# Kernel optimization log

Hardware: AMD Instinct MI355X
Metric: run time of the kernel (lower is better)

Reference implementation:

```python
import jax, jax.numpy as jnp
import numpy as np

N, D, V = 4096, 1024, 50257


def setup_inputs() -> dict:
    key = jax.random.key(0)
    kx, kw, kt = jax.random.split(key, 3)
    x = jax.random.normal(kx, (N, D), dtype=jnp.float32)
    weight = jax.random.normal(kw, (V, D), dtype=jnp.float32) * 0.02
    target = jax.random.randint(kt, (N,), 0, V, dtype=jnp.int64)
    return {"x": x, "weight": weight, "target": target}


def reference(x, weight, target):
    # fused fc -> log_softmax -> nll_loss (mean reduction)
    logits = jnp.einsum("nd,vd->nv", x, weight)          # [N, V]
    logp = jax.nn.log_softmax(logits, axis=-1)            # stable log-softmax
    nll = -jnp.take_along_axis(logp, target[:, None].astype(jnp.int32), axis=-1)[:, 0]
    return jnp.mean(nll)
```

## Files before the change

kernel.cpp:

```cpp
#include <hip/hip_runtime.h>
#include <hip/hip_bf16.h>
#include <stdint.h>

#define NROWS 4096
#define DDIM  1024
#define VDIM  50257
#define VPAD  50304
#define NVT   393
#define NMT   16

#define DESCALE (1.0f / 512.0f)

#define PITCH  80
#define B_BASE 20480
#define STAGE  30720

typedef long  i64;
typedef i64   i64x2 __attribute__((ext_vector_type(2)));
typedef int   i32x4 __attribute__((ext_vector_type(4)));
typedef int   i32x8 __attribute__((ext_vector_type(8)));
typedef float f32x16 __attribute__((ext_vector_type(16)));

#define SCALE1 0x7F7F7F7F

__device__ __forceinline__ i32x8 ld_frag(const unsigned char* p) {
  i32x4 lo = *(const i32x4*)p;
  i32x4 hi = *(const i32x4*)(p + 16);
  return __builtin_shufflevector(lo, hi, 0, 1, 2, 3, 4, 5, 6, 7);
}

__global__ __launch_bounds__(256)
void cvtq_kernel(const float* __restrict__ src, uint32_t* __restrict__ dst,
                 size_t n_src, float scale) {
  size_t i = ((size_t)blockIdx.x * 256 + threadIdx.x) * 16;
  uint32_t o[4] = {0u, 0u, 0u, 0u};
  if (i < n_src) {
    const float4* s = (const float4*)(src + i);
    #pragma unroll
    for (int d = 0; d < 4; ++d) {
      float4 f = s[d];
      uint32_t v = 0;
      v = __builtin_amdgcn_cvt_pk_fp8_f32(f.x * scale, f.y * scale, v, false);
      v = __builtin_amdgcn_cvt_pk_fp8_f32(f.z * scale, f.w * scale, v, true);
      o[d] = v;
    }
  }
  *(uint4*)(dst + i / 4) = make_uint4(o[0], o[1], o[2], o[3]);
}

__global__ __launch_bounds__(256)
void tlogit_kernel(const float* __restrict__ x, const float* __restrict__ w,
                   const int* __restrict__ tgt, float* __restrict__ lt) {
  int n = blockIdx.x;
  int t = tgt[n];
  const float4* xr = (const float4*)(x + (size_t)n * DDIM);
  const float4* wr = (const float4*)(w + (size_t)t * DDIM);
  float4 a = xr[threadIdx.x];
  float4 b = wr[threadIdx.x];
  float s = a.x * b.x + a.y * b.y + a.z * b.z + a.w * b.w;
  #pragma unroll
  for (int m = 32; m; m >>= 1) s += __shfl_down(s, m);
  __shared__ float red[4];
  if ((threadIdx.x & 63) == 0) red[threadIdx.x >> 6] = s;
  __syncthreads();
  if (threadIdx.x == 0) lt[n] = red[0] + red[1] + red[2] + red[3];
}

__global__ __launch_bounds__(256, 2)
void gemm_lse_kernel(const uint8_t* __restrict__ xq,
                     const uint8_t* __restrict__ wq,
                     float* __restrict__ S) {
  __shared__ __align__(16) unsigned char smem[2 * STAGE];

  const int tid  = threadIdx.x;
  const int wid  = tid >> 6;
  const int lane = tid & 63;
  const int c31  = lane & 31;
  const int h    = lane >> 5;

  const int flat = blockIdx.x + blockIdx.y * 16;
  int bm, vt;
  if (flat >= (NVT - 1) * 16) { vt = NVT - 1; bm = flat - (NVT - 1) * 16; }
  else { vt = (flat >> 7) * 8 + (flat & 7); bm = (flat >> 3) & 15; }
  const int m0 = bm * 256;
  const int v0 = vt * 128;

  const int wave_m = wid >> 1;
  const int wave_n = wid & 1;

  const int lr = lane >> 2;
  const int lc = lane & 3;
  const uint8_t* gA[4]; uint32_t wAo[4];
  #pragma unroll
  for (int a = 0; a < 4; ++a) {
    int r = (wid * 4 + a) * 16 + lr;
    gA[a]  = xq + (size_t)(m0 + r) * DDIM + lc * 16;
    wAo[a] = (uint32_t)(r * PITCH + lc * 16);
  }
  const uint8_t* gB[2]; uint32_t wBo[2];
  #pragma unroll
  for (int b = 0; b < 2; ++b) {
    int r = (wid * 2 + b) * 16 + lr;
    gB[b]  = wq + (size_t)(v0 + r) * DDIM + lc * 16;
    wBo[b] = (uint32_t)(B_BASE + r * PITCH + lc * 16);
  }

  uint32_t aoff[4], boff[2];
  #pragma unroll
  for (int mi = 0; mi < 4; ++mi)
    aoff[mi] = (uint32_t)((wave_m * 128 + mi * 32 + c31) * PITCH + h * 32);
  #pragma unroll
  for (int ni = 0; ni < 2; ++ni)
    boff[ni] = (uint32_t)(B_BASE + (wave_n * 64 + ni * 32 + c31) * PITCH + h * 32);

  f32x16 acc[4][2] = {};
  i64x2 rA[4], rB[2];

  #pragma unroll
  for (int a = 0; a < 4; ++a) rA[a] = *(const i64x2*)gA[a];
  #pragma unroll
  for (int b = 0; b < 2; ++b) rB[b] = *(const i64x2*)gB[b];
  #pragma unroll
  for (int a = 0; a < 4; ++a) *(i64x2*)(smem + wAo[a]) = rA[a];
  #pragma unroll
  for (int b = 0; b < 2; ++b) *(i64x2*)(smem + wBo[b]) = rB[b];
  #pragma unroll
  for (int a = 0; a < 4; ++a) rA[a] = *(const i64x2*)(gA[a] + 64);
  #pragma unroll
  for (int b = 0; b < 2; ++b) rB[b] = *(const i64x2*)(gB[b] + 64);
  __syncthreads();

  #pragma unroll 2
  for (int k = 0; k < 16; ++k) {
    const uint32_t sb = (uint32_t)(k & 1) * STAGE;
    const uint32_t nb = STAGE - sb;

    if (k + 1 < 16) {
      #pragma unroll
      for (int a = 0; a < 4; ++a) *(i64x2*)(smem + nb + wAo[a]) = rA[a];
      #pragma unroll
      for (int b = 0; b < 2; ++b) *(i64x2*)(smem + nb + wBo[b]) = rB[b];
    }
    if (k + 2 < 16) {
      #pragma unroll
      for (int a = 0; a < 4; ++a) rA[a] = *(const i64x2*)(gA[a] + (k + 2) * 64);
      #pragma unroll
      for (int b = 0; b < 2; ++b) rB[b] = *(const i64x2*)(gB[b] + (k + 2) * 64);
    }

    __builtin_amdgcn_sched_barrier(0);

    i32x8 bf0 = ld_frag(smem + sb + boff[0]);
    i32x8 bf1 = ld_frag(smem + sb + boff[1]);
    #pragma unroll
    for (int mi = 0; mi < 4; ++mi) {
      i32x8 afm = ld_frag(smem + sb + aoff[mi]);
      acc[mi][0] = __builtin_amdgcn_mfma_scale_f32_32x32x64_f8f6f4(
          afm, bf0, acc[mi][0], 0, 0, 0, SCALE1, 0, SCALE1);
      acc[mi][1] = __builtin_amdgcn_mfma_scale_f32_32x32x64_f8f6f4(
          afm, bf1, acc[mi][1], 0, 0, 0, SCALE1, 0, SCALE1);
    }

    __syncthreads();
  }

  #pragma unroll
  for (int mi = 0; mi < 4; ++mi) {
    #pragma unroll
    for (int r = 0; r < 16; ++r) {
      float pacc = 0.f;
      #pragma unroll
      for (int ni = 0; ni < 2; ++ni) {
        int v = v0 + wave_n * 64 + ni * 32 + c31;
        float e = __expf(acc[mi][ni][r] * DESCALE);
        pacc += (v < VDIM) ? e : 0.f;
      }
      pacc += __shfl_xor(pacc, 16);
      pacc += __shfl_xor(pacc, 8);
      pacc += __shfl_xor(pacc, 4);
      pacc += __shfl_xor(pacc, 2);
      pacc += __shfl_xor(pacc, 1);
      if (c31 == 0) {
        int row = m0 + wave_m * 128 + mi * 32 + (r & 3) + 8 * (r >> 2) + 4 * h;
        atomicAdd(&S[row], pacc);
      }
    }
  }
}

__global__ __launch_bounds__(1024)
void loss_kernel(const float* __restrict__ S, const float* __restrict__ lt,
                 float* __restrict__ out) {
  float s = 0.f;
  for (int n = threadIdx.x; n < NROWS; n += 1024)
    s += logf(S[n]) - lt[n];
  #pragma unroll
  for (int m = 32; m; m >>= 1) s += __shfl_down(s, m);
  __shared__ float red[16];
  if ((threadIdx.x & 63) == 0) red[threadIdx.x >> 6] = s;
  __syncthreads();
  if (threadIdx.x == 0) {
    float t = 0.f;
    #pragma unroll
    for (int i = 0; i < 16; ++i) t += red[i];
    out[0] = t / (float)NROWS;
  }
}

extern "C" void kernel_launch(void* const* d_in, const int* in_sizes, int n_in,
                              void* d_out, int out_size, void* d_ws, size_t ws_size,
                              hipStream_t stream) {
  const float* x = (const float*)d_in[0];
  const float* w = (const float*)d_in[1];
  const int*   t = (const int*)d_in[2];
  float* out = (float*)d_out;

  char* ws = (char*)d_ws;
  const size_t wq_bytes = (size_t)VPAD * DDIM;
  const size_t xq_bytes = (size_t)NROWS * DDIM;
  uint8_t* wq = (uint8_t*)ws;
  uint8_t* xq = (uint8_t*)(ws + wq_bytes);
  float*   S  = (float*)(ws + wq_bytes + xq_bytes);
  float*   lt = S + NROWS;

  if (ws_size < wq_bytes + xq_bytes + 2 * NROWS * sizeof(float)) return;

  hipMemsetAsync(S, 0, NROWS * sizeof(float), stream);
  cvtq_kernel<<<VPAD / 4, 256, 0, stream>>>(w, (uint32_t*)wq,
                                            (size_t)VDIM * DDIM, 64.0f);
  cvtq_kernel<<<NROWS / 4, 256, 0, stream>>>(x, (uint32_t*)xq,
                                             (size_t)NROWS * DDIM, 8.0f);
  tlogit_kernel<<<NROWS, 256, 0, stream>>>(x, w, t, lt);

  dim3 grid(NMT, NVT);
  gemm_lse_kernel<<<grid, 256, 0, stream>>>(xq, wq, S);

  loss_kernel<<<1, 1024, 0, stream>>>(S, lt, out);
}
```

Baseline: 690.0 us.

## Pre-swizzle FP8 operands into MFMA fragment order and drop LDS staging

The quantization kernels now write x and weight in a fragment-major layout, so each lane's 32-byte MFMA operand is contiguous in global memory. The GEMM reads fragments straight from global/L2 and no longer uses shared memory, double buffering or block barriers. This removes LDS store/load traffic and syncs. In exchange, waves that share an operand tile each fetch it separately with no reuse through LDS, and the loop has no explicit prefetch, so it depends on L2 bandwidth and on hiding global-load latency.

```diff
diff --git a/kernel.cpp b/kernel.cpp
--- a/kernel.cpp
+++ b/kernel.cpp
@@ -11,10 +11,6 @@
 
 #define DESCALE (1.0f / 512.0f)
 
-#define PITCH  80
-#define B_BASE 20480
-#define STAGE  30720
-
 typedef long  i64;
 typedef i64   i64x2 __attribute__((ext_vector_type(2)));
 typedef int   i32x4 __attribute__((ext_vector_type(4)));
@@ -23,21 +19,25 @@
 
 #define SCALE1 0x7F7F7F7F
 
-__device__ __forceinline__ i32x8 ld_frag(const unsigned char* p) {
+__device__ __forceinline__ i32x8 ld_gfrag(const uint8_t* p) {
   i32x4 lo = *(const i32x4*)p;
   i32x4 hi = *(const i32x4*)(p + 16);
   return __builtin_shufflevector(lo, hi, 0, 1, 2, 3, 4, 5, 6, 7);
 }
 
 __global__ __launch_bounds__(256)
-void cvtq_kernel(const float* __restrict__ src, uint32_t* __restrict__ dst,
-                 size_t n_src, float scale) {
-  size_t i = ((size_t)blockIdx.x * 256 + threadIdx.x) * 16;
-  uint32_t o[4] = {0u, 0u, 0u, 0u};
-  if (i < n_src) {
-    const float4* s = (const float4*)(src + i);
+void cvtq_frag_kernel(const float* __restrict__ src, uint32_t* __restrict__ dst,
+                      int nrows_valid, float scale) {
+  int t = blockIdx.x * 256 + threadIdx.x;
+  int l  = t & 63;
+  int gc = t >> 6;
+  int row = (gc >> 4) * 32 + (l & 31);
+  int col = (gc & 15) * 64 + (l >> 5) * 32;
+  uint32_t o[8] = {0u,0u,0u,0u,0u,0u,0u,0u};
+  if (row < nrows_valid) {
+    const float4* s = (const float4*)(src + (size_t)row * DDIM + col);
     #pragma unroll
-    for (int d = 0; d < 4; ++d) {
+    for (int d = 0; d < 8; ++d) {
       float4 f = s[d];
       uint32_t v = 0;
       v = __builtin_amdgcn_cvt_pk_fp8_f32(f.x * scale, f.y * scale, v, false);
@@ -45,7 +45,9 @@
       o[d] = v;
     }
   }
-  *(uint4*)(dst + i / 4) = make_uint4(o[0], o[1], o[2], o[3]);
+  uint4* dp = (uint4*)(dst + (size_t)t * 8);
+  dp[0] = make_uint4(o[0], o[1], o[2], o[3]);
+  dp[1] = make_uint4(o[4], o[5], o[6], o[7]);
 }
 
 __global__ __launch_bounds__(256)
@@ -67,11 +69,9 @@
 }
 
 __global__ __launch_bounds__(256, 2)
-void gemm_lse_kernel(const uint8_t* __restrict__ xq,
-                     const uint8_t* __restrict__ wq,
+void gemm_lse_kernel(const uint8_t* __restrict__ xqf,
+                     const uint8_t* __restrict__ wqf,
                      float* __restrict__ S) {
-  __shared__ __align__(16) unsigned char smem[2 * STAGE];
-
   const int tid  = threadIdx.x;
   const int wid  = tid >> 6;
   const int lane = tid & 63;
@@ -88,80 +88,30 @@
   const int wave_m = wid >> 1;
   const int wave_n = wid & 1;
 
-  const int lr = lane >> 2;
-  const int lc = lane & 3;
-  const uint8_t* gA[4]; uint32_t wAo[4];
-  #pragma unroll
-  for (int a = 0; a < 4; ++a) {
-    int r = (wid * 4 + a) * 16 + lr;
-    gA[a]  = xq + (size_t)(m0 + r) * DDIM + lc * 16;
-    wAo[a] = (uint32_t)(r * PITCH + lc * 16);
-  }
-  const uint8_t* gB[2]; uint32_t wBo[2];
-  #pragma unroll
-  for (int b = 0; b < 2; ++b) {
-    int r = (wid * 2 + b) * 16 + lr;
-    gB[b]  = wq + (size_t)(v0 + r) * DDIM + lc * 16;
-    wBo[b] = (uint32_t)(B_BASE + r * PITCH + lc * 16);
-  }
-
-  uint32_t aoff[4], boff[2];
+  const uint8_t* pA[4];
   #pragma unroll
   for (int mi = 0; mi < 4; ++mi)
-    aoff[mi] = (uint32_t)((wave_m * 128 + mi * 32 + c31) * PITCH + h * 32);
+    pA[mi] = xqf + ((size_t)(bm * 8 + wave_m * 4 + mi) * 16) * 2048 + lane * 32;
+  const uint8_t* pB[2];
   #pragma unroll
   for (int ni = 0; ni < 2; ++ni)
-    boff[ni] = (uint32_t)(B_BASE + (wave_n * 64 + ni * 32 + c31) * PITCH + h * 32);
+    pB[ni] = wqf + ((size_t)(vt * 4 + wave_n * 2 + ni) * 16) * 2048 + lane * 32;
 
   f32x16 acc[4][2] = {};
-  i64x2 rA[4], rB[2];
 
-  #pragma unroll
-  for (int a = 0; a < 4; ++a) rA[a] = *(const i64x2*)gA[a];
-  #pragma unroll
-  for (int b = 0; b < 2; ++b) rB[b] = *(const i64x2*)gB[b];
-  #pragma unroll
-  for (int a = 0; a < 4; ++a) *(i64x2*)(smem + wAo[a]) = rA[a];
-  #pragma unroll
-  for (int b = 0; b < 2; ++b) *(i64x2*)(smem + wBo[b]) = rB[b];
-  #pragma unroll
-  for (int a = 0; a < 4; ++a) rA[a] = *(const i64x2*)(gA[a] + 64);
-  #pragma unroll
-  for (int b = 0; b < 2; ++b) rB[b] = *(const i64x2*)(gB[b] + 64);
-  __syncthreads();
-
-  #pragma unroll 2
-  for (int k = 0; k < 16; ++k) {
-    const uint32_t sb = (uint32_t)(k & 1) * STAGE;
-    const uint32_t nb = STAGE - sb;
-
-    if (k + 1 < 16) {
-      #pragma unroll
-      for (int a = 0; a < 4; ++a) *(i64x2*)(smem + nb + wAo[a]) = rA[a];
-      #pragma unroll
-      for (int b = 0; b < 2; ++b) *(i64x2*)(smem + nb + wBo[b]) = rB[b];
-    }
-    if (k + 2 < 16) {
-      #pragma unroll
-      for (int a = 0; a < 4; ++a) rA[a] = *(const i64x2*)(gA[a] + (k + 2) * 64);
-      #pragma unroll
-      for (int b = 0; b < 2; ++b) rB[b] = *(const i64x2*)(gB[b] + (k + 2) * 64);
-    }
-
-    __builtin_amdgcn_sched_barrier(0);
-
-    i32x8 bf0 = ld_frag(smem + sb + boff[0]);
-    i32x8 bf1 = ld_frag(smem + sb + boff[1]);
+  #pragma unroll 1
+  for (int c = 0; c < 16; ++c) {
+    const size_t co = (size_t)c * 2048;
+    i32x8 bf0 = ld_gfrag(pB[0] + co);
+    i32x8 bf1 = ld_gfrag(pB[1] + co);
     #pragma unroll
     for (int mi = 0; mi < 4; ++mi) {
-      i32x8 afm = ld_frag(smem + sb + aoff[mi]);
+      i32x8 afm = ld_gfrag(pA[mi] + co);
       acc[mi][0] = __builtin_amdgcn_mfma_scale_f32_32x32x64_f8f6f4(
           afm, bf0, acc[mi][0], 0, 0, 0, SCALE1, 0, SCALE1);
       acc[mi][1] = __builtin_amdgcn_mfma_scale_f32_32x32x64_f8f6f4(
           afm, bf1, acc[mi][1], 0, 0, 0, SCALE1, 0, SCALE1);
     }
-
-    __syncthreads();
   }
 
   #pragma unroll
@@ -218,22 +168,22 @@
   char* ws = (char*)d_ws;
   const size_t wq_bytes = (size_t)VPAD * DDIM;
   const size_t xq_bytes = (size_t)NROWS * DDIM;
-  uint8_t* wq = (uint8_t*)ws;
-  uint8_t* xq = (uint8_t*)(ws + wq_bytes);
-  float*   S  = (float*)(ws + wq_bytes + xq_bytes);
-  float*   lt = S + NROWS;
+  uint8_t* wqf = (uint8_t*)ws;
+  uint8_t* xqf = (uint8_t*)(ws + wq_bytes);
+  float*   S   = (float*)(ws + wq_bytes + xq_bytes);
+  float*   lt  = S + NROWS;
 
   if (ws_size < wq_bytes + xq_bytes + 2 * NROWS * sizeof(float)) return;
 
   hipMemsetAsync(S, 0, NROWS * sizeof(float), stream);
-  cvtq_kernel<<<VPAD / 4, 256, 0, stream>>>(w, (uint32_t*)wq,
-                                            (size_t)VDIM * DDIM, 64.0f);
-  cvtq_kernel<<<NROWS / 4, 256, 0, stream>>>(x, (uint32_t*)xq,
-                                             (size_t)NROWS * DDIM, 8.0f);
+  cvtq_frag_kernel<<<VPAD / 8, 256, 0, stream>>>(w, (uint32_t*)wqf,
+                                                 VDIM, 64.0f);
+  cvtq_frag_kernel<<<NROWS / 8, 256, 0, stream>>>(x, (uint32_t*)xqf,
+                                                  NROWS, 8.0f);
   tlogit_kernel<<<NROWS, 256, 0, stream>>>(x, w, t, lt);
 
   dim3 grid(NMT, NVT);
-  gemm_lse_kernel<<<grid, 256, 0, stream>>>(xq, wq, S);
+  gemm_lse_kernel<<<grid, 256, 0, stream>>>(xqf, wqf, S);
 
   loss_kernel<<<1, 1024, 0, stream>>>(S, lt, out);
 }
```

After: 664.6 us. 3.7% less time.
